# Optimization experiments

Measured on AMD Instinct MI355X. Metric: run time of the kernel, lower is better.

Reference implementation:

```python
import jax, jax.numpy as jnp
import numpy as np

B, SQ, SK = 32, 512, 512
Q_DIM = 512
K_DIM = 512
H = 8
HD = 64
INNER = H * HD
MAX_POS = 512
SCALE = 1.0 / np.sqrt(HD)


def setup_inputs() -> dict:
    key = jax.random.key(0)
    ks = jax.random.split(key, 10)
    query = jax.random.normal(ks[0], (B, SQ, Q_DIM), dtype=jnp.float32)
    key_t = jax.random.normal(ks[1], (B, SK, K_DIM), dtype=jnp.float32)
    value = jax.random.normal(ks[2], (B, SK, K_DIM), dtype=jnp.float32)
    mask = jax.random.randint(ks[3], (B, SQ, SK), 0, 2, dtype=jnp.int32)
    # learned parameters (Linear weights stored as [in, out]; to_q/k/v have no bias)
    Wq = jax.random.normal(ks[4], (Q_DIM, INNER), dtype=jnp.float32) * 0.02
    Wk = jax.random.normal(ks[5], (K_DIM, INNER), dtype=jnp.float32) * 0.02
    Wv = jax.random.normal(ks[6], (K_DIM, INNER), dtype=jnp.float32) * 0.02
    Wo = jax.random.normal(ks[7], (INNER, Q_DIM), dtype=jnp.float32) * 0.02
    bo = jnp.zeros((Q_DIM,), dtype=jnp.float32)
    rel_pos_emb = jax.random.normal(ks[8], (MAX_POS, MAX_POS), dtype=jnp.float32) * 0.02
    return {"query": query, "key": key_t, "value": value, "mask": mask,
            "Wq": Wq, "Wk": Wk, "Wv": Wv, "Wo": Wo, "bo": bo,
            "rel_pos_emb": rel_pos_emb}


def reference(query, key, value, mask, Wq, Wk, Wv, Wo, bo, rel_pos_emb):
    # Projections (no bias for q/k/v)
    q = query @ Wq   # [B, SQ, INNER]
    k = key @ Wk     # [B, SK, INNER]
    v = value @ Wv   # [B, SK, INNER]
    # split heads -> [B, H, S, HD]
    q = q.reshape(B, SQ, H, HD).transpose(0, 2, 1, 3)
    k = k.reshape(B, SK, H, HD).transpose(0, 2, 1, 3)
    v = v.reshape(B, SK, H, HD).transpose(0, 2, 1, 3)
    # scaled scores + learned relative-position bias (shared across batch/heads)
    scores = jnp.einsum('bhqd,bhkd->bhqk', q, k) * SCALE
    bias = rel_pos_emb[:SQ, :SK]          # [SQ, SK]
    scores = scores + bias[None, None, :, :]
    # additive masking: positions where mask == 0 get -inf
    scores = jnp.where(mask[:, None, :, :] == 0, -jnp.inf, scores)
    attn = jax.nn.softmax(scores, axis=-1)
    # dropout is identity in eval mode (p treated as inference)
    out = jnp.einsum('bhqk,bhkd->bhqd', attn, v)
    out = out.transpose(0, 2, 1, 3).reshape(B, SQ, INNER)
    return out @ Wo + bo
```

## Files before the change

kernel.cpp:

```cpp
#include <hip/hip_runtime.h>
#include <stdint.h>


typedef unsigned short u16;
typedef __attribute__((ext_vector_type(4))) float f32x4;
typedef __attribute__((ext_vector_type(8))) __bf16 bf16x8;
typedef __attribute__((ext_vector_type(4))) unsigned short u16x4;
typedef __attribute__((ext_vector_type(8))) unsigned short u16x8;
typedef __attribute__((ext_vector_type(4))) int i32x4;
typedef __attribute__((ext_vector_type(4))) _Float16 f16x4;
typedef __attribute__((ext_vector_type(8))) _Float16 f16x8;

#define MFMA16(a, b, c) __builtin_amdgcn_mfma_f32_16x16x32_bf16((a), (b), (c), 0, 0, 0)

#define LGKM0_BARRIER()                                        \
  do {                                                         \
    asm volatile("s_waitcnt lgkmcnt(0)" ::: "memory");         \
    __builtin_amdgcn_s_barrier();                              \
    __builtin_amdgcn_sched_barrier(0);                         \
  } while (0)

__device__ __forceinline__ u16 f2bf(float f) {
  unsigned u = __float_as_uint(f);
  u += 0x7fffu + ((u >> 16) & 1u);
  return (u16)(u >> 16);
}
__device__ __forceinline__ float bf2f(u16 h) {
  return __uint_as_float(((unsigned)h) << 16);
}

__device__ __forceinline__ void gl_lds16(const void* g, void* l) {
  __builtin_amdgcn_global_load_lds(
      (const __attribute__((address_space(1))) unsigned int*)g,
      (__attribute__((address_space(3))) unsigned int*)l, 16, 0, 0);
}

__global__ __launch_bounds__(256) void k_prep(
    const float* __restrict__ Wq, const float* __restrict__ Wk,
    const float* __restrict__ Wv, const float* __restrict__ Wo,
    u16* __restrict__ Wt, u16* __restrict__ WoHi, u16* __restrict__ WoLo) {
  int idx = blockIdx.x * 256 + threadIdx.x;
  int n = idx >> 9, k = idx & 511;
  int src = k * 512 + n;
  Wt[idx]          = f2bf(Wq[src]);
  Wt[262144 + idx] = f2bf(Wk[src]);
  Wt[524288 + idx] = f2bf(Wv[src]);
  float wo = Wo[src];
  u16 hi = f2bf(wo);
  WoHi[idx] = hi;
  WoLo[idx] = f2bf(wo - bf2f(hi));
}

__global__ __launch_bounds__(256) void k_mb(
    const int* __restrict__ mask, const float* __restrict__ bias,
    _Float16* __restrict__ MB) {
  size_t i8 = ((size_t)blockIdx.x * 256 + threadIdx.x) * 8;
  i32x4 m0 = *(const i32x4*)&mask[i8];
  i32x4 m1 = *(const i32x4*)&mask[i8 + 4];
  size_t bi = i8 & 262143;
  f32x4 b0 = *(const f32x4*)&bias[bi];
  f32x4 b1 = *(const f32x4*)&bias[bi + 4];
  const _Float16 MASKED = (_Float16)(-60000.0f);
  f16x8 o;
#pragma unroll
  for (int e = 0; e < 4; ++e) {
    o[e]     = (m0[e] != 0) ? (_Float16)b0[e] : MASKED;
    o[e + 4] = (m1[e] != 0) ? (_Float16)b1[e] : MASKED;
  }
  *(f16x8*)&MB[i8] = o;
}

__global__ __launch_bounds__(256, 4) void k_proj(
    const float* __restrict__ Xq, const float* __restrict__ Xk, const float* __restrict__ Xv,
    const u16* __restrict__ Wt,
    u16* __restrict__ Qb, u16* __restrict__ Kb, u16* __restrict__ Vtb) {
  __shared__ __align__(16) u16 lA[2][64][40];
  const int mat = blockIdx.z;
  const float* __restrict__ A = (mat == 0) ? Xq : (mat == 1) ? Xk : Xv;
  const u16* __restrict__ Bw = Wt + (size_t)mat * 262144;
  const int tid = threadIdx.x, lane = tid & 63, wn = tid >> 6;
  const int m0 = blockIdx.y * 64, n0 = blockIdx.x * 256;
  const int fr = lane & 15, g = lane >> 4;
  const int arow = tid >> 2, acg = tid & 3;
  const float* __restrict__ Ar = &A[(size_t)(m0 + arow) * 512 + acg * 8];
  const u16* __restrict__ Bp[4];
#pragma unroll
  for (int fn = 0; fn < 4; ++fn)
    Bp[fn] = &Bw[(size_t)(n0 + wn * 64 + fn * 16 + fr) * 512 + g * 8];

  f32x4 acc[4][4] = {};
  f32x4 va[2][2];
  bf16x8 bB[4];

  {
    f32x4 v0 = *(const f32x4*)&Ar[0];
    f32x4 v1 = *(const f32x4*)&Ar[4];
    va[0][0] = *(const f32x4*)&Ar[32];
    va[0][1] = *(const f32x4*)&Ar[36];
    u16x8 hv;
#pragma unroll
    for (int e = 0; e < 4; ++e) { hv[e] = f2bf(v0[e]); hv[e + 4] = f2bf(v1[e]); }
    *(u16x8*)&lA[0][arow][acg * 8] = hv;
  }
  LGKM0_BARRIER();

#pragma unroll
  for (int kt = 0; kt < 16; ++kt) {
    const int cur = kt & 1, nxt = cur ^ 1;
    const int k0 = kt * 32;
#pragma unroll
    for (int fn = 0; fn < 4; ++fn)
      bB[fn] = *(const bf16x8*)(Bp[fn] + k0);
    if (kt < 14) {
      va[nxt][0] = *(const f32x4*)&Ar[(kt + 2) * 32];
      va[nxt][1] = *(const f32x4*)&Ar[(kt + 2) * 32 + 4];
    }
#pragma unroll
    for (int fm = 0; fm < 4; ++fm) {
      bf16x8 af = *(const bf16x8*)&lA[cur][fm * 16 + fr][g * 8];
#pragma unroll
      for (int fn = 0; fn < 4; ++fn)
        acc[fm][fn] = MFMA16(af, bB[fn], acc[fm][fn]);
    }
    if (kt < 15) {
      u16x8 hv;
#pragma unroll
      for (int e = 0; e < 4; ++e) {
        hv[e]     = f2bf(va[cur][0][e]);
        hv[e + 4] = f2bf(va[cur][1][e]);
      }
      *(u16x8*)&lA[nxt][arow][acg * 8] = hv;
    }
    LGKM0_BARRIER();
  }

  if (mat < 2) {
    u16* __restrict__ Out = (mat == 0) ? Qb : Kb;
#pragma unroll
    for (int fm = 0; fm < 4; ++fm) {
#pragma unroll
      for (int fn = 0; fn < 4; ++fn) {
        int gn = n0 + wn * 64 + fn * 16 + fr;
        int hh = gn >> 6, hd = gn & 63;
#pragma unroll
        for (int r = 0; r < 4; ++r) {
          int gm = m0 + fm * 16 + g * 4 + r;
          int b = gm >> 9, sq = gm & 511;
          Out[(size_t)((b * 8 + hh) * 512 + sq) * 64 + hd] = f2bf(acc[fm][fn][r]);
        }
      }
    }
  } else {
#pragma unroll
    for (int fm = 0; fm < 4; ++fm) {
      int gm0 = m0 + fm * 16 + g * 4;
      int b = gm0 >> 9, sq0 = gm0 & 511;
#pragma unroll
      for (int fn = 0; fn < 4; ++fn) {
        int gn = n0 + wn * 64 + fn * 16 + fr;
        int hh = gn >> 6, hd = gn & 63;
        u16x4 pv;
        pv[0] = f2bf(acc[fm][fn][0]); pv[1] = f2bf(acc[fm][fn][1]);
        pv[2] = f2bf(acc[fm][fn][2]); pv[3] = f2bf(acc[fm][fn][3]);
        *(u16x4*)&Vtb[(size_t)((b * 8 + hh) * 64 + hd) * 512 + sq0] = pv;
      }
    }
  }
}

__global__ __launch_bounds__(256, 4) void k_attn(
    const u16* __restrict__ Qb, const u16* __restrict__ Kb, const u16* __restrict__ Vtb,
    const _Float16* __restrict__ MB, float* __restrict__ Obuf) {
  __shared__ __align__(16) u16 kbuf[2][64][64];
  __shared__ __align__(16) u16 vbuf[2][64][64];
  __shared__ __align__(16) u16 lP[4][16][64];
  const int tid = threadIdx.x, lane = tid & 63, w = tid >> 6;
  const int orig = blockIdx.x;
  const int xcd = orig & 7, idx = orig >> 3;
  const int qq = idx & 3, h = (idx >> 2) & 7;
  const int b = xcd + 8 * (idx >> 5);
  const int bh = b * 8 + h;
  const int fr = lane & 15, g = lane >> 4;
  const int sq0 = qq * 128 + w * 32;
  const int sw = (fr & 7) << 4;
  const u16* __restrict__ Qh = Qb + (size_t)bh * 32768;
  const u16* __restrict__ Kh = Kb + (size_t)bh * 32768;
  const u16* __restrict__ Vh = Vtb + (size_t)bh * 32768;
  const _Float16* __restrict__ MBr = MB + (size_t)b * 262144 + (size_t)(sq0 + fr) * 512;
  char* lProw = (char*)&lP[w][fr][0];
  const char* kcb;
  const char* vcb;

  const int sub = lane >> 3;
  const int xo = ((lane & 7) ^ sub) * 8;

  bf16x8 qf[2][2];
#pragma unroll
  for (int qfi = 0; qfi < 2; ++qfi)
#pragma unroll
    for (int kc = 0; kc < 2; ++kc)
      qf[qfi][kc] = *(const bf16x8*)&Qh[(size_t)(sq0 + qfi * 16 + fr) * 64 + kc * 32 + g * 8];

  f32x4 oacc[2][4] = {};
  float mrow[2] = {-1e30f, -1e30f}, lrow[2] = {0.f, 0.f};

  {
    if (w < 2) {
      const int rb = w * 32;
      const u16* gs = Kh + (size_t)(rb + sub) * 64 + xo;
#pragma unroll
      for (int i = 0; i < 4; ++i)
        gl_lds16(gs + (size_t)i * 8 * 64, &kbuf[0][rb + i * 8][0]);
    } else {
      const int rb = (w - 2) * 32;
      const u16* gs = Vh + (size_t)(rb + sub) * 512 + xo;
#pragma unroll
      for (int i = 0; i < 4; ++i)
        gl_lds16(gs + (size_t)i * 8 * 512, &vbuf[0][rb + i * 8][0]);
    }
  }
  __syncthreads();

  int cur = 0;
  for (int kt = 0; kt < 8; ++kt) {
    const int sk0 = kt * 64;
    f16x4 mbv[2][4];
#pragma unroll
    for (int qfi = 0; qfi < 2; ++qfi)
#pragma unroll
      for (int fn = 0; fn < 4; ++fn)
        mbv[qfi][fn] = *(const f16x4*)&MBr[(size_t)qfi * 16 * 512 + sk0 + fn * 16 + g * 4];
    if (kt < 7) {
      const int nb = cur ^ 1, sk0n = sk0 + 64;
      if (w < 2) {
        const int rb = w * 32;
        const u16* gs = Kh + (size_t)(sk0n + rb + sub) * 64 + xo;
#pragma unroll
        for (int i = 0; i < 4; ++i)
          gl_lds16(gs + (size_t)i * 8 * 64, &kbuf[nb][rb + i * 8][0]);
      } else {
        const int rb = (w - 2) * 32;
        const u16* gs = Vh + (size_t)(rb + sub) * 512 + sk0n + xo;
#pragma unroll
        for (int i = 0; i < 4; ++i)
          gl_lds16(gs + (size_t)i * 8 * 512, &vbuf[nb][rb + i * 8][0]);
      }
    }
    kcb = (const char*)kbuf[cur];
    vcb = (const char*)vbuf[cur];
    f32x4 sacc[2][4] = {};
#pragma unroll
    for (int fn = 0; fn < 4; ++fn) {
      const int r = fn * 16 + fr;
      bf16x8 kf0 = *(const bf16x8*)(kcb + (size_t)r * 128 + ((0 * 64 + g * 16) ^ sw));
      bf16x8 kf1 = *(const bf16x8*)(kcb + (size_t)r * 128 + ((1 * 64 + g * 16) ^ sw));
      sacc[0][fn] = MFMA16(kf0, qf[0][0], sacc[0][fn]);
      sacc[0][fn] = MFMA16(kf1, qf[0][1], sacc[0][fn]);
      sacc[1][fn] = MFMA16(kf0, qf[1][0], sacc[1][fn]);
      sacc[1][fn] = MFMA16(kf1, qf[1][1], sacc[1][fn]);
    }
#pragma unroll
    for (int qfi = 0; qfi < 2; ++qfi)
#pragma unroll
      for (int fn = 0; fn < 4; ++fn)
#pragma unroll
        for (int r = 0; r < 4; ++r)
          sacc[qfi][fn][r] = sacc[qfi][fn][r] * 0.125f + (float)mbv[qfi][fn][r];

#pragma unroll
    for (int qfi = 0; qfi < 2; ++qfi) {
      float t0 = fmaxf(fmaxf(sacc[qfi][0][0], sacc[qfi][0][1]),
                       fmaxf(sacc[qfi][0][2], sacc[qfi][0][3]));
      float t1 = fmaxf(fmaxf(sacc[qfi][1][0], sacc[qfi][1][1]),
                       fmaxf(sacc[qfi][1][2], sacc[qfi][1][3]));
      float t2 = fmaxf(fmaxf(sacc[qfi][2][0], sacc[qfi][2][1]),
                       fmaxf(sacc[qfi][2][2], sacc[qfi][2][3]));
      float t3 = fmaxf(fmaxf(sacc[qfi][3][0], sacc[qfi][3][1]),
                       fmaxf(sacc[qfi][3][2], sacc[qfi][3][3]));
      float pm = fmaxf(fmaxf(t0, t1), fmaxf(t2, t3));
      pm = fmaxf(pm, __shfl_xor(pm, 16));
      pm = fmaxf(pm, __shfl_xor(pm, 32));
      if (!__all(pm - mrow[qfi] <= 8.0f)) {
        float mn = fmaxf(mrow[qfi], pm);
        float sfac = __expf(mrow[qfi] - mn);
        mrow[qfi] = mn;
        lrow[qfi] *= sfac;
#pragma unroll
        for (int r = 0; r < 4; ++r) {
          float sr = __shfl(sfac, g * 4 + r);
#pragma unroll
          for (int fnh = 0; fnh < 4; ++fnh)
            oacc[qfi][fnh][r] *= sr;
        }
      }
      float ps = 0.f;
#pragma unroll
      for (int fn = 0; fn < 4; ++fn) {
        float p0 = __expf(sacc[qfi][fn][0] - mrow[qfi]);
        float p1 = __expf(sacc[qfi][fn][1] - mrow[qfi]);
        float p2 = __expf(sacc[qfi][fn][2] - mrow[qfi]);
        float p3 = __expf(sacc[qfi][fn][3] - mrow[qfi]);
        ps += (p0 + p1) + (p2 + p3);
        u16x4 pw;
        pw[0] = f2bf(p0); pw[1] = f2bf(p1); pw[2] = f2bf(p2); pw[3] = f2bf(p3);
        *(u16x4*)(lProw + ((fn * 32 + g * 8) ^ sw)) = pw;
      }
      ps += __shfl_xor(ps, 16);
      ps += __shfl_xor(ps, 32);
      lrow[qfi] += ps;
      __builtin_amdgcn_wave_barrier();
#pragma unroll
      for (int kc = 0; kc < 2; ++kc) {
        bf16x8 pf = *(const bf16x8*)(lProw + ((kc * 64 + g * 16) ^ sw));
#pragma unroll
        for (int fnh = 0; fnh < 4; ++fnh) {
          const int vr = fnh * 16 + fr;
          bf16x8 vf = *(const bf16x8*)(vcb + (size_t)vr * 128 + ((kc * 64 + g * 16) ^ sw));
          oacc[qfi][fnh] = MFMA16(pf, vf, oacc[qfi][fnh]);
        }
      }
      __builtin_amdgcn_wave_barrier();
    }
    __syncthreads();
    cur ^= 1;
  }
#pragma unroll
  for (int qfi = 0; qfi < 2; ++qfi) {
#pragma unroll
    for (int r = 0; r < 4; ++r) {
      float lr = __shfl(lrow[qfi], g * 4 + r);
      float inv = 1.0f / lr;
      const int sq = sq0 + qfi * 16 + g * 4 + r;
      float* orow = &Obuf[((size_t)b * 512 + sq) * 512 + h * 64];
#pragma unroll
      for (int fnh = 0; fnh < 4; ++fnh)
        orow[fnh * 16 + fr] = oacc[qfi][fnh][r] * inv;
    }
  }
}

__global__ __launch_bounds__(512, 4) void k_out(
    const float* __restrict__ Oin, const u16* __restrict__ WoHi, const u16* __restrict__ WoLo,
    const float* __restrict__ bo, float* __restrict__ out) {
  __shared__ __align__(16) u16 lAh[2][64][40], lAl[2][64][40];
  const int tid = threadIdx.x, lane = tid & 63, wn = tid >> 6;
  const int m0 = blockIdx.y * 64, n0 = blockIdx.x * 256;
  const int fr = lane & 15, g = lane >> 4;
  const int arow = tid >> 3, acg = tid & 7;
  const float* __restrict__ Ar = &Oin[(size_t)(m0 + arow) * 512 + acg * 4];
  const u16* __restrict__ Bh[2];
  const u16* __restrict__ Bl[2];
#pragma unroll
  for (int fn = 0; fn < 2; ++fn) {
    size_t row = (size_t)(n0 + wn * 32 + fn * 16 + fr) * 512 + g * 8;
    Bh[fn] = &WoHi[row];
    Bl[fn] = &WoLo[row];
  }

  f32x4 acc[4][2] = {};
  f32x4 va[2];

  {
    f32x4 v = *(const f32x4*)&Ar[0];
    va[0] = *(const f32x4*)&Ar[32];
    u16x4 hv, lv;
#pragma unroll
    for (int e = 0; e < 4; ++e) {
      u16 hb = f2bf(v[e]);
      hv[e] = hb;
      lv[e] = f2bf(v[e] - bf2f(hb));
    }
    *(u16x4*)&lAh[0][arow][acg * 4] = hv;
    *(u16x4*)&lAl[0][arow][acg * 4] = lv;
  }
  LGKM0_BARRIER();

#pragma unroll
  for (int kt = 0; kt < 16; ++kt) {
    const int cur = kt & 1, nxt = cur ^ 1;
    const int k0 = kt * 32;
    bf16x8 bh[2], bl[2];
#pragma unroll
    for (int fn = 0; fn < 2; ++fn) {
      bh[fn] = *(const bf16x8*)(Bh[fn] + k0);
      bl[fn] = *(const bf16x8*)(Bl[fn] + k0);
    }
    if (kt < 14)
      va[nxt] = *(const f32x4*)&Ar[(kt + 2) * 32];
#pragma unroll
    for (int fm = 0; fm < 4; ++fm) {
      bf16x8 ah = *(const bf16x8*)&lAh[cur][fm * 16 + fr][g * 8];
      bf16x8 al = *(const bf16x8*)&lAl[cur][fm * 16 + fr][g * 8];
#pragma unroll
      for (int fn = 0; fn < 2; ++fn) {
        acc[fm][fn] = MFMA16(ah, bh[fn], acc[fm][fn]);
        acc[fm][fn] = MFMA16(ah, bl[fn], acc[fm][fn]);
        acc[fm][fn] = MFMA16(al, bh[fn], acc[fm][fn]);
      }
    }
    if (kt < 15) {
      u16x4 hv, lv;
#pragma unroll
      for (int e = 0; e < 4; ++e) {
        u16 hb = f2bf(va[cur][e]);
        hv[e] = hb;
        lv[e] = f2bf(va[cur][e] - bf2f(hb));
      }
      *(u16x4*)&lAh[nxt][arow][acg * 4] = hv;
      *(u16x4*)&lAl[nxt][arow][acg * 4] = lv;
    }
    LGKM0_BARRIER();
  }

#pragma unroll
  for (int fm = 0; fm < 4; ++fm) {
#pragma unroll
    for (int fn = 0; fn < 2; ++fn) {
      int gn = n0 + wn * 32 + fn * 16 + fr;
      float bv = bo[gn];
#pragma unroll
      for (int r = 0; r < 4; ++r) {
        int gm = m0 + fm * 16 + g * 4 + r;
        out[(size_t)gm * 512 + gn] = acc[fm][fn][r] + bv;
      }
    }
  }
}

extern "C" void kernel_launch(void* const* d_in, const int* in_sizes, int n_in,
                              void* d_out, int out_size, void* d_ws, size_t ws_size,
                              hipStream_t stream) {
  (void)in_sizes; (void)n_in; (void)out_size; (void)ws_size;
  const float* query = (const float*)d_in[0];
  const float* key_t = (const float*)d_in[1];
  const float* value = (const float*)d_in[2];
  const int*   mask  = (const int*)d_in[3];
  const float* Wq    = (const float*)d_in[4];
  const float* Wk    = (const float*)d_in[5];
  const float* Wv    = (const float*)d_in[6];
  const float* Wo    = (const float*)d_in[7];
  const float* bo    = (const float*)d_in[8];
  const float* bias  = (const float*)d_in[9];
  float* out = (float*)d_out;

  char* p = (char*)d_ws;
  u16* Wt   = (u16*)p; p += (size_t)3 * 512 * 512 * 2;
  u16* WoHi = (u16*)p; p += (size_t)512 * 512 * 2;
  u16* WoLo = (u16*)p; p += (size_t)512 * 512 * 2;
  u16* Qb   = (u16*)p; p += (size_t)32 * 8 * 512 * 64 * 2;
  u16* Kb   = (u16*)p; p += (size_t)32 * 8 * 512 * 64 * 2;
  u16* Vtb  = (u16*)p; p += (size_t)32 * 8 * 512 * 64 * 2;
  float* Obuf = (float*)p; p += (size_t)32 * 512 * 512 * 4;
  _Float16* MBp = (_Float16*)p;

  k_prep<<<1024, 256, 0, stream>>>(Wq, Wk, Wv, Wo, Wt, WoHi, WoLo);
  k_mb<<<4096, 256, 0, stream>>>(mask, bias, MBp);
  k_proj<<<dim3(2, 256, 3), 256, 0, stream>>>(query, key_t, value, Wt, Qb, Kb, Vtb);
  k_attn<<<1024, 256, 0, stream>>>(Qb, Kb, Vtb, MBp, Obuf);
  k_out<<<dim3(2, 256), 512, 0, stream>>>(Obuf, WoHi, WoLo, bo, out);
}
```

Before: 189.8 us.

## Pre-convert activations to bf16 and stream projection tiles via direct global-to-LDS loads

Adds a separate kernel that converts query/key/value to bf16 into a buffer aliased with Obuf, so the projection GEMM no longer converts fp32 in registers. The projection kernel now uses 512-thread blocks covering 128 rows, loads A tiles straight into XOR-swizzled LDS with gl_lds16, and steps through K in chunks of 64. This removes per-tile conversion work and halves how often B weights are reloaded per row. In exchange it adds a full extra pass that writes and rereads the activations through global memory, and it relies on k_mb being reordered so the shared buffer is safe to reuse.

```diff
diff --git a/kernel.cpp b/kernel.cpp
--- a/kernel.cpp
+++ b/kernel.cpp
@@ -51,6 +51,23 @@
   WoLo[idx] = f2bf(wo - bf2f(hi));
 }
 
+__global__ __launch_bounds__(256) void k_cvt(
+    const float* __restrict__ Xq, const float* __restrict__ Xk,
+    const float* __restrict__ Xv, u16* __restrict__ Xb) {
+  const float* __restrict__ src =
+      (blockIdx.y == 0) ? Xq : (blockIdx.y == 1) ? Xk : Xv;
+  size_t i8 = ((size_t)blockIdx.x * 256 + threadIdx.x) * 8;
+  f32x4 v0 = *(const f32x4*)&src[i8];
+  f32x4 v1 = *(const f32x4*)&src[i8 + 4];
+  u16x8 o;
+#pragma unroll
+  for (int e = 0; e < 4; ++e) {
+    o[e]     = f2bf(v0[e]);
+    o[e + 4] = f2bf(v1[e]);
+  }
+  *(u16x8*)&Xb[(size_t)blockIdx.y * 8388608 + i8] = o;
+}
+
 __global__ __launch_bounds__(256) void k_mb(
     const int* __restrict__ mask, const float* __restrict__ bias,
     _Float16* __restrict__ MB) {
@@ -70,68 +87,65 @@
   *(f16x8*)&MB[i8] = o;
 }
 
-__global__ __launch_bounds__(256, 4) void k_proj(
-    const float* __restrict__ Xq, const float* __restrict__ Xk, const float* __restrict__ Xv,
-    const u16* __restrict__ Wt,
+__global__ __launch_bounds__(512, 4) void k_proj(
+    const u16* __restrict__ Xb, const u16* __restrict__ Wt,
     u16* __restrict__ Qb, u16* __restrict__ Kb, u16* __restrict__ Vtb) {
-  __shared__ __align__(16) u16 lA[2][64][40];
+  __shared__ __align__(16) u16 lAb[2][128][64];
   const int mat = blockIdx.z;
-  const float* __restrict__ A = (mat == 0) ? Xq : (mat == 1) ? Xk : Xv;
+  const u16* __restrict__ Ab = Xb + (size_t)mat * 8388608;
   const u16* __restrict__ Bw = Wt + (size_t)mat * 262144;
-  const int tid = threadIdx.x, lane = tid & 63, wn = tid >> 6;
-  const int m0 = blockIdx.y * 64, n0 = blockIdx.x * 256;
+  const int tid = threadIdx.x, lane = tid & 63, wid = tid >> 6;
+  const int wm = wid >> 2, wn = wid & 3;
+  const int m0 = blockIdx.y * 128, n0 = blockIdx.x * 256;
   const int fr = lane & 15, g = lane >> 4;
-  const int arow = tid >> 2, acg = tid & 3;
-  const float* __restrict__ Ar = &A[(size_t)(m0 + arow) * 512 + acg * 8];
+
+  const int sub = lane >> 3;
+  const int xo = ((lane & 7) ^ sub) * 8;
+  const int swr = (fr & 7) << 4;
+
   const u16* __restrict__ Bp[4];
 #pragma unroll
   for (int fn = 0; fn < 4; ++fn)
     Bp[fn] = &Bw[(size_t)(n0 + wn * 64 + fn * 16 + fr) * 512 + g * 8];
 
   f32x4 acc[4][4] = {};
-  f32x4 va[2][2];
-  bf16x8 bB[4];
-
-  {
-    f32x4 v0 = *(const f32x4*)&Ar[0];
-    f32x4 v1 = *(const f32x4*)&Ar[4];
-    va[0][0] = *(const f32x4*)&Ar[32];
-    va[0][1] = *(const f32x4*)&Ar[36];
-    u16x8 hv;
-#pragma unroll
-    for (int e = 0; e < 4; ++e) { hv[e] = f2bf(v0[e]); hv[e + 4] = f2bf(v1[e]); }
-    *(u16x8*)&lA[0][arow][acg * 8] = hv;
-  }
-  LGKM0_BARRIER();
-
-#pragma unroll
-  for (int kt = 0; kt < 16; ++kt) {
+
+#pragma unroll
+  for (int p = 0; p < 2; ++p) {
+    const int rb = p * 64 + wid * 8;
+    gl_lds16(Ab + (size_t)(m0 + rb + sub) * 512 + xo, &lAb[0][rb][0]);
+  }
+  __syncthreads();
+
+  for (int kt = 0; kt < 8; ++kt) {
     const int cur = kt & 1, nxt = cur ^ 1;
-    const int k0 = kt * 32;
-#pragma unroll
-    for (int fn = 0; fn < 4; ++fn)
-      bB[fn] = *(const bf16x8*)(Bp[fn] + k0);
-    if (kt < 14) {
-      va[nxt][0] = *(const f32x4*)&Ar[(kt + 2) * 32];
-      va[nxt][1] = *(const f32x4*)&Ar[(kt + 2) * 32 + 4];
-    }
-#pragma unroll
-    for (int fm = 0; fm < 4; ++fm) {
-      bf16x8 af = *(const bf16x8*)&lA[cur][fm * 16 + fr][g * 8];
-#pragma unroll
-      for (int fn = 0; fn < 4; ++fn)
-        acc[fm][fn] = MFMA16(af, bB[fn], acc[fm][fn]);
-    }
-    if (kt < 15) {
-      u16x8 hv;
-#pragma unroll
-      for (int e = 0; e < 4; ++e) {
-        hv[e]     = f2bf(va[cur][0][e]);
-        hv[e + 4] = f2bf(va[cur][1][e]);
-      }
-      *(u16x8*)&lA[nxt][arow][acg * 8] = hv;
-    }
-    LGKM0_BARRIER();
+    const int k0 = kt * 64;
+    bf16x8 bB[2][4];
+#pragma unroll
+    for (int fn = 0; fn < 4; ++fn) {
+      bB[0][fn] = *(const bf16x8*)(Bp[fn] + k0);
+      bB[1][fn] = *(const bf16x8*)(Bp[fn] + k0 + 32);
+    }
+    if (kt < 7) {
+#pragma unroll
+      for (int p = 0; p < 2; ++p) {
+        const int rb = p * 64 + wid * 8;
+        gl_lds16(Ab + (size_t)(m0 + rb + sub) * 512 + k0 + 64 + xo,
+                 &lAb[nxt][rb][0]);
+      }
+    }
+#pragma unroll
+    for (int kc = 0; kc < 2; ++kc) {
+#pragma unroll
+      for (int fm = 0; fm < 4; ++fm) {
+        const char* rowb = (const char*)&lAb[cur][wm * 64 + fm * 16 + fr][0];
+        bf16x8 af = *(const bf16x8*)(rowb + ((kc * 64 + g * 16) ^ swr));
+#pragma unroll
+        for (int fn = 0; fn < 4; ++fn)
+          acc[fm][fn] = MFMA16(af, bB[kc][fn], acc[fm][fn]);
+      }
+    }
+    __syncthreads();
   }
 
   if (mat < 2) {
@@ -144,7 +158,7 @@
         int hh = gn >> 6, hd = gn & 63;
 #pragma unroll
         for (int r = 0; r < 4; ++r) {
-          int gm = m0 + fm * 16 + g * 4 + r;
+          int gm = m0 + wm * 64 + fm * 16 + g * 4 + r;
           int b = gm >> 9, sq = gm & 511;
           Out[(size_t)((b * 8 + hh) * 512 + sq) * 64 + hd] = f2bf(acc[fm][fn][r]);
         }
@@ -153,7 +167,7 @@
   } else {
 #pragma unroll
     for (int fm = 0; fm < 4; ++fm) {
-      int gm0 = m0 + fm * 16 + g * 4;
+      int gm0 = m0 + wm * 64 + fm * 16 + g * 4;
       int b = gm0 >> 9, sq0 = gm0 & 511;
 #pragma unroll
       for (int fn = 0; fn < 4; ++fn) {
@@ -450,12 +464,14 @@
   u16* Qb   = (u16*)p; p += (size_t)32 * 8 * 512 * 64 * 2;
   u16* Kb   = (u16*)p; p += (size_t)32 * 8 * 512 * 64 * 2;
   u16* Vtb  = (u16*)p; p += (size_t)32 * 8 * 512 * 64 * 2;
-  float* Obuf = (float*)p; p += (size_t)32 * 512 * 512 * 4;
-  _Float16* MBp = (_Float16*)p;
+  u16* Xb = (u16*)p;
+  float* Obuf = (float*)p;
+  _Float16* MBp = (_Float16*)(p + (size_t)32 * 512 * 512 * 4);
 
   k_prep<<<1024, 256, 0, stream>>>(Wq, Wk, Wv, Wo, Wt, WoHi, WoLo);
+  k_cvt<<<dim3(4096, 3), 256, 0, stream>>>(query, key_t, value, Xb);
+  k_proj<<<dim3(2, 128, 3), 512, 0, stream>>>(Xb, Wt, Qb, Kb, Vtb);
   k_mb<<<4096, 256, 0, stream>>>(mask, bias, MBp);
-  k_proj<<<dim3(2, 256, 3), 256, 0, stream>>>(query, key_t, value, Wt, Qb, Kb, Vtb);
   k_attn<<<1024, 256, 0, stream>>>(Qb, Kb, Vtb, MBp, Obuf);
   k_out<<<dim3(2, 256), 512, 0, stream>>>(Obuf, WoHi, WoLo, bo, out);
 }
```

Result: slower. 194.3 us (+2.4%).
